# Kernel optimization log

Measured on AMD Instinct MI355X. Metric: run time of the kernel, lower is better.

The kernel has to match this reference:

```python
import jax, jax.numpy as jnp
import numpy as np

B, T, N_EMBD, H = 8, 2048, 1024, 128

def setup_inputs() -> dict:
    key = jax.random.key(0)
    k1, k2, k3, k4 = jax.random.split(key, 4)
    x = jax.random.normal(k1, (B, T, N_EMBD), dtype=jnp.float32)
    s = 1.0 / np.sqrt(N_EMBD).astype(np.float32)
    Wq = jax.random.normal(k2, (N_EMBD, H), dtype=jnp.float32) * s
    Wk = jax.random.normal(k3, (N_EMBD, H), dtype=jnp.float32) * s
    Wv = jax.random.normal(k4, (N_EMBD, H), dtype=jnp.float32) * s
    return {"x": x, "Wq": Wq, "Wk": Wk, "Wv": Wv}

def reference(x, Wq, Wk, Wv):
    # x: [B,T,C]; projections (no bias per init_kwargs)
    q = x @ Wq  # [B,T,H]
    k = x @ Wk  # [B,T,H]
    v = x @ Wv  # [B,T,H]
    scale = jnp.asarray(k.shape[-1], x.dtype) ** -0.5
    att = jnp.einsum('bth,bsh->bts', q, k) * scale  # [B,T,T]
    Tlen = x.shape[1]
    causal = jnp.tril(jnp.ones((Tlen, Tlen), dtype=bool))  # bias buffer tril mask
    att = jnp.where(causal, att, jnp.asarray(-jnp.inf, att.dtype))
    att = jax.nn.softmax(att, axis=-1)
    # dropout omitted (eval mode / deterministic reference)
    y = jnp.einsum('bts,bsh->bth', att, v)  # [B,T,H]
    return y
```

## Files before the change

kernel.cpp:

```cpp
#include <hip/hip_runtime.h>
#include <hip/hip_bf16.h>
#include <stdint.h>

#define BB 8
#define TT 2048
#define CC 1024
#define HH 128
#define VTP 2112

typedef __attribute__((ext_vector_type(8))) short bf16x8;
typedef __attribute__((ext_vector_type(8))) unsigned short u16x8;
typedef __attribute__((ext_vector_type(4))) float f32x4;
typedef __attribute__((ext_vector_type(8))) _Float16 h16x8;

static __device__ __forceinline__ unsigned short f2bf(float f) {
    union { float f; uint32_t u; } v; v.f = f;
    return (unsigned short)((v.u + 0x7fffu + ((v.u >> 16) & 1u)) >> 16);
}

#define GLOBAL_AS __attribute__((address_space(1)))
#define LDS_AS    __attribute__((address_space(3)))
static __device__ __forceinline__ void async16(const void* g, void* l) {
    __builtin_amdgcn_global_load_lds((const GLOBAL_AS void*)g, (LDS_AS void*)l, 16, 0, 0);
}

__global__ __launch_bounds__(256) void wconv(
    const float* __restrict__ Wq, const float* __restrict__ Wk,
    const float* __restrict__ Wv, unsigned short* __restrict__ Wb)
{
    int u = blockIdx.x * 256 + threadIdx.x;
    if (u >= 3 * 128 * 128) return;
    int kc = u & 127, n = (u >> 7) & 127, mat = u >> 14;
    const float* W = (mat == 0) ? Wq : (mat == 1) ? Wk : Wv;
    const float* s = W + (size_t)(kc * 8) * HH + n;
    u16x8 v;
    #pragma unroll
    for (int j = 0; j < 8; j++) v[j] = f2bf(s[(size_t)j * HH]);
    *(u16x8*)(Wb + ((size_t)mat * HH + n) * CC + kc * 8) = v;
}

#define BS_U16 2304
#define EQ_OFF 0
#define EK_OFF 4352
#define EV_OFF 8704
__global__ __launch_bounds__(256) void qkv_proj(
    const float* __restrict__ x, const unsigned short* __restrict__ Wb,
    unsigned short* __restrict__ Q, unsigned short* __restrict__ K,
    unsigned short* __restrict__ Vt)
{
    __shared__ __align__(16) unsigned short lds[26880];

    const int m0  = blockIdx.x * 32;
    const int tid = threadIdx.x;
    const int lane = tid & 63;
    const int w    = tid >> 6;
    const int qd   = lane >> 4;
    const int ln   = lane & 15;

    f32x4 acc[2][6];
    #pragma unroll
    for (int i = 0; i < 2; i++)
        #pragma unroll
        for (int j = 0; j < 6; j++) acc[i][j] = (f32x4){0.f,0.f,0.f,0.f};

    const int xr = tid >> 3;
    const int xg = (tid & 7) * 8;

    float4 xf[2];
    {
        const float* s = x + (size_t)(m0 + xr) * CC + xg;
        xf[0] = ((const float4*)s)[0];
        xf[1] = ((const float4*)s)[1];
    }

    for (int k0 = 0; k0 < CC; k0 += 64) {
        {
            u16x8 v0;
            v0[0]=f2bf(xf[0].x); v0[1]=f2bf(xf[0].y); v0[2]=f2bf(xf[0].z); v0[3]=f2bf(xf[0].w);
            v0[4]=f2bf(xf[1].x); v0[5]=f2bf(xf[1].y); v0[6]=f2bf(xf[1].z); v0[7]=f2bf(xf[1].w);
            *(u16x8*)&lds[xr * 72 + xg] = v0;
        }
        #pragma unroll
        for (int i = 0; i < 12; i++) {
            int sb = i * 256 + w * 64;
            int slot = sb + lane;
            int row = slot >> 3, j = (slot & 7) ^ (row & 7);
            async16(Wb + (size_t)row * CC + k0 + j * 8, &lds[BS_U16 + sb * 8]);
        }
        __syncthreads();
        if (k0 + 64 < CC) {
            const float* s = x + (size_t)(m0 + xr) * CC + k0 + 64 + xg;
            xf[0] = ((const float4*)s)[0];
            xf[1] = ((const float4*)s)[1];
        }
        #pragma unroll
        for (int ks = 0; ks < 2; ks++) {
            bf16x8 a0 = *(const bf16x8*)&lds[ln * 72 + ks*32 + qd*8];
            bf16x8 a1 = *(const bf16x8*)&lds[(16 + ln) * 72 + ks*32 + qd*8];
            #pragma unroll
            for (int nf = 0; nf < 6; nf++) {
                int row = w * 96 + nf * 16 + ln;
                int ch  = (ks * 4 + qd) ^ (row & 7);
                bf16x8 b = *(const bf16x8*)&lds[BS_U16 + (row * 8 + ch) * 8];
                acc[0][nf] = __builtin_amdgcn_mfma_f32_16x16x32_bf16(a0, b, acc[0][nf], 0, 0, 0);
                acc[1][nf] = __builtin_amdgcn_mfma_f32_16x16x32_bf16(a1, b, acc[1][nf], 0, 0, 0);
            }
        }
        __syncthreads();
    }

    #pragma unroll
    for (int mf = 0; mf < 2; mf++)
        #pragma unroll
        for (int nf = 0; nf < 6; nf++) {
            int n = w * 96 + nf * 16;
            int mat = n >> 7, hb = n & 127;
            #pragma unroll
            for (int r = 0; r < 4; r++) {
                unsigned short v = f2bf(acc[mf][nf][r]);
                int mrow = mf*16 + qd*4 + r;
                if (mat < 2) lds[(mat ? EK_OFF : EQ_OFF) + mrow * 136 + hb + ln] = v;
                else         lds[EV_OFF + (hb + ln) * 40 + mrow] = v;
            }
        }
    __syncthreads();
    {
        int rr = tid >> 3, c0 = (tid & 7) * 16;
        #pragma unroll
        for (int i = 0; i < 2; i++) {
            u16x8 vq = *(const u16x8*)&lds[EQ_OFF + rr * 136 + c0 + i * 8];
            *(u16x8*)(Q + (size_t)(m0 + rr) * HH + c0 + i * 8) = vq;
            u16x8 vk = *(const u16x8*)&lds[EK_OFF + rr * 136 + c0 + i * 8];
            *(u16x8*)(K + (size_t)(m0 + rr) * HH + c0 + i * 8) = vk;
        }
    }
    {
        int bb = m0 >> 11, t0 = m0 & (TT - 1);
        int hh = tid >> 1, tf = (tid & 1) * 16;
        #pragma unroll
        for (int i = 0; i < 2; i++) {
            u16x8 vv = *(const u16x8*)&lds[EV_OFF + hh * 40 + tf + i * 8];
            *(u16x8*)(Vt + ((size_t)bb * HH + hh) * VTP + t0 + tf + i * 8) = vv;
        }
    }
}

__global__ __launch_bounds__(256) void attn(
    const unsigned short* __restrict__ Q, const unsigned short* __restrict__ K,
    const unsigned short* __restrict__ Vt, float* __restrict__ out)
{
    __shared__ __align__(16) unsigned short Ks[2][64 * 128];
    __shared__ __align__(16) unsigned short Vs[2][128 * 64];
    __shared__ __align__(16) unsigned short Ps[4][16 * 40];
    __shared__ float Lp[4][16];

    const int tid  = threadIdx.x;
    const int lane = tid & 63;
    const int wave = tid >> 6;
    const int qd = lane >> 4;
    const int ln = lane & 15;
    const int qgrp  = wave >> 1;
    const int khalf = wave & 1;

    const int bx = blockIdx.x;
    int b, qt;
    if (bx < 256) { b = bx & 7;               qt = 63 - (bx >> 3); }
    else          { int u = bx - 256; b = u & 7; qt = u >> 3; }
    const int qbase = qt * 32 + qgrp * 16;
    const int nst = (qt + 2) >> 1;

    const unsigned short* Qb = Q  + (size_t)b * TT * HH;
    const unsigned short* Kb = K  + (size_t)b * TT * HH;
    const unsigned short* Vb = Vt + (size_t)b * HH * VTP;

    bf16x8 aq[4];
    #pragma unroll
    for (int c = 0; c < 4; c++)
        aq[c] = *(const bf16x8*)(Qb + (size_t)(qbase + ln) * HH + c * 32 + qd * 8);

    f32x4 O[8];
    float lsum[4];
    #pragma unroll
    for (int h = 0; h < 8; h++) O[h] = (f32x4){0.f,0.f,0.f,0.f};
    #pragma unroll
    for (int r = 0; r < 4; r++) lsum[r] = 0.f;

    const float sl   = 0.08838834764831843f * 1.4426950408889634f;
    const float M0L2 = 7.2134752044448f;
    unsigned short* ps = Ps[wave];

    #define STAGE(S0, BUF)                                                          \
        do {                                                                        \
            _Pragma("unroll")                                                       \
            for (int i = 0; i < 4; i++) {                                           \
                int sb = i * 256 + wave * 64;                                       \
                int slot = sb + lane;                                               \
                int row = slot >> 4, jj = (slot & 15) ^ (row & 15);                 \
                async16(Kb + (size_t)((S0) + row) * HH + jj * 8, &Ks[BUF][sb * 8]); \
            }                                                                       \
            _Pragma("unroll")                                                       \
            for (int i = 0; i < 4; i++) {                                           \
                int sb = i * 256 + wave * 64;                                       \
                int slot = sb + lane;                                               \
                int row = slot >> 3, jj = (slot & 7) ^ (row & 7);                   \
                async16(Vb + (size_t)row * VTP + (S0) + jj * 8, &Vs[BUF][sb * 8]);  \
            }                                                                       \
        } while (0)

    STAGE(0, 0);
    for (int st = 0; st < nst; st++) {
        __syncthreads();
        const int buf = st & 1;
        if (st + 1 < nst) STAGE((st + 1) * 64, buf ^ 1);
        const int s0 = st * 64;

        f32x4 s[2] = {(f32x4){0.f,0.f,0.f,0.f}, (f32x4){0.f,0.f,0.f,0.f}};
        #pragma unroll
        for (int nt = 0; nt < 2; nt++) {
            int krow = khalf * 32 + nt * 16;
            #pragma unroll
            for (int c = 0; c < 4; c++) {
                bf16x8 bk = *(const bf16x8*)&Ks[buf][(krow + ln) * 128 + ((c*4 + qd) ^ ln) * 8];
                s[nt] = __builtin_amdgcn_mfma_f32_16x16x32_bf16(aq[c], bk, s[nt], 0, 0, 0);
            }
        }
        #pragma unroll
        for (int nt = 0; nt < 2; nt++) {
            int col = s0 + khalf * 32 + nt * 16 + ln;
            #pragma unroll
            for (int r = 0; r < 4; r++) {
                int row = qbase + qd * 4 + r;
                float e = __builtin_amdgcn_exp2f(s[nt][r] * sl - M0L2);
                e = (col <= row) ? e : 0.f;
                lsum[r] += e;
                ps[(qd*4 + r) * 40 + nt*16 + ln] = f2bf(e);
            }
        }
        bf16x8 ap = *(const bf16x8*)&ps[ln * 40 + qd * 8];
        #pragma unroll
        for (int ht = 0; ht < 8; ht++) {
            int vrow = ht * 16 + ln;
            bf16x8 bv = *(const bf16x8*)&Vs[buf][vrow * 64 + ((khalf*4 + qd) ^ (vrow & 7)) * 8];
            O[ht] = __builtin_amdgcn_mfma_f32_16x16x32_bf16(ap, bv, O[ht], 0, 0, 0);
        }
    }

    __syncthreads();
    #pragma unroll
    for (int r = 0; r < 4; r++) {
        float sum = lsum[r];
        #pragma unroll
        for (int off = 1; off < 16; off <<= 1)
            sum += __shfl_xor(sum, off, 64);
        if (ln == 0) Lp[wave][qd*4 + r] = sum;
    }
    _Float16* om = (_Float16*)&Ks[0][0] + (size_t)wave * 16 * 128;
    #pragma unroll
    for (int ht = 0; ht < 8; ht++)
        #pragma unroll
        for (int r = 0; r < 4; r++)
            om[(qd*4 + r) * 128 + ht*16 + ln] = (_Float16)O[ht][r];
    __syncthreads();

    {
        int row = tid >> 3, h0 = (tid & 7) * 16;
        int g = row >> 4, q = row & 15;
        float L = Lp[2*g][q] + Lp[2*g + 1][q];
        float inv = 1.0f / L;
        const _Float16* p0 = (const _Float16*)&Ks[0][0] + (size_t)(2*g) * 2048 + q * 128 + h0;
        const _Float16* p1 = p0 + 2048;
        float* op = out + ((size_t)b * TT + qt * 32 + row) * HH + h0;
        #pragma unroll
        for (int i = 0; i < 4; i++) {
            float4 v;
            v.x = ((float)p0[i*4+0] + (float)p1[i*4+0]) * inv;
            v.y = ((float)p0[i*4+1] + (float)p1[i*4+1]) * inv;
            v.z = ((float)p0[i*4+2] + (float)p1[i*4+2]) * inv;
            v.w = ((float)p0[i*4+3] + (float)p1[i*4+3]) * inv;
            ((float4*)op)[i] = v;
        }
    }
    #undef STAGE
}

extern "C" void kernel_launch(void* const* d_in, const int* in_sizes, int n_in,
                              void* d_out, int out_size, void* d_ws, size_t ws_size,
                              hipStream_t stream) {
    const float* x  = (const float*)d_in[0];
    const float* Wq = (const float*)d_in[1];
    const float* Wk = (const float*)d_in[2];
    const float* Wv = (const float*)d_in[3];

    unsigned short* Wb = (unsigned short*)d_ws;
    unsigned short* Qw = Wb + (size_t)3 * HH * CC;
    unsigned short* Kw = Qw + (size_t)BB * TT * HH;
    unsigned short* Vw = Kw + (size_t)BB * TT * HH;

    wconv<<<dim3(192), 256, 0, stream>>>(Wq, Wk, Wv, Wb);
    qkv_proj<<<dim3(512), 256, 0, stream>>>(x, Wb, Qw, Kw, Vw);
    attn<<<dim3(512), 256, 0, stream>>>(Qw, Kw, Vw, (float*)d_out);
}
```

Baseline: 160.5 us.

## Split attention key range across four waves per query group, drop double buffering

The attention block grows from 256 to 512 threads, so each 16-row query group is processed by four waves instead of two, each covering a 32-key slice of a 128-key stage. K/V tiles are loaded once per 128-key stage into a single LDS buffer with a barrier before compute, replacing the previous double-buffered prefetch of 64-key stages. The epilogue sums four partial outputs and row sums. This halves the number of stages and raises the wave count per block, but gives up overlap of loads with compute and adds an extra barrier per stage. It also computes more fully masked work on the diagonal stage.

Measured after the change: 153.6 us. -4.3%, faster.

```diff
diff --git a/kernel.cpp b/kernel.cpp
--- a/kernel.cpp
+++ b/kernel.cpp
@@ -145,29 +145,30 @@
     }
 }
 
-__global__ __launch_bounds__(256) void attn(
+__global__ __launch_bounds__(512) void attn(
     const unsigned short* __restrict__ Q, const unsigned short* __restrict__ K,
     const unsigned short* __restrict__ Vt, float* __restrict__ out)
 {
-    __shared__ __align__(16) unsigned short Ks[2][64 * 128];
-    __shared__ __align__(16) unsigned short Vs[2][128 * 64];
-    __shared__ __align__(16) unsigned short Ps[4][16 * 40];
-    __shared__ float Lp[4][16];
+    __shared__ __align__(16) unsigned short Ks[128 * 128];
+    __shared__ __align__(16) unsigned short Vs[128 * 128];
+    __shared__ __align__(16) unsigned short Ps[8][16 * 40];
+    __shared__ float Lp[8][16];
 
     const int tid  = threadIdx.x;
     const int lane = tid & 63;
     const int wave = tid >> 6;
     const int qd = lane >> 4;
     const int ln = lane & 15;
-    const int qgrp  = wave >> 1;
-    const int khalf = wave & 1;
+    const int qgrp = wave >> 2;
+    const int kq   = wave & 2 ? (wave & 3) : (wave & 3);
+    const int kq4  = wave & 3;
 
     const int bx = blockIdx.x;
     int b, qt;
     if (bx < 256) { b = bx & 7;               qt = 63 - (bx >> 3); }
     else          { int u = bx - 256; b = u & 7; qt = u >> 3; }
     const int qbase = qt * 32 + qgrp * 16;
-    const int nst = (qt + 2) >> 1;
+    const int nst = (qt + 4) >> 2;
 
     const unsigned short* Qb = Q  + (size_t)b * TT * HH;
     const unsigned short* Kb = K  + (size_t)b * TT * HH;
@@ -189,44 +190,37 @@
     const float M0L2 = 7.2134752044448f;
     unsigned short* ps = Ps[wave];
 
-    #define STAGE(S0, BUF)                                                          \
-        do {                                                                        \
-            _Pragma("unroll")                                                       \
-            for (int i = 0; i < 4; i++) {                                           \
-                int sb = i * 256 + wave * 64;                                       \
-                int slot = sb + lane;                                               \
-                int row = slot >> 4, jj = (slot & 15) ^ (row & 15);                 \
-                async16(Kb + (size_t)((S0) + row) * HH + jj * 8, &Ks[BUF][sb * 8]); \
-            }                                                                       \
-            _Pragma("unroll")                                                       \
-            for (int i = 0; i < 4; i++) {                                           \
-                int sb = i * 256 + wave * 64;                                       \
-                int slot = sb + lane;                                               \
-                int row = slot >> 3, jj = (slot & 7) ^ (row & 7);                   \
-                async16(Vb + (size_t)row * VTP + (S0) + jj * 8, &Vs[BUF][sb * 8]);  \
-            }                                                                       \
-        } while (0)
-
-    STAGE(0, 0);
     for (int st = 0; st < nst; st++) {
+        const int s0 = st * 128;
+        #pragma unroll
+        for (int i = 0; i < 4; i++) {
+            int sb = i * 512 + wave * 64;
+            int slot = sb + lane;
+            int row = slot >> 4, jj = (slot & 15) ^ (row & 15);
+            async16(Kb + (size_t)(s0 + row) * HH + jj * 8, &Ks[sb * 8]);
+        }
+        #pragma unroll
+        for (int i = 0; i < 4; i++) {
+            int sb = i * 512 + wave * 64;
+            int slot = sb + lane;
+            int row = slot >> 4, jj = (slot & 15) ^ (row & 15);
+            async16(Vb + (size_t)row * VTP + s0 + jj * 8, &Vs[sb * 8]);
+        }
         __syncthreads();
-        const int buf = st & 1;
-        if (st + 1 < nst) STAGE((st + 1) * 64, buf ^ 1);
-        const int s0 = st * 64;
 
         f32x4 s[2] = {(f32x4){0.f,0.f,0.f,0.f}, (f32x4){0.f,0.f,0.f,0.f}};
         #pragma unroll
         for (int nt = 0; nt < 2; nt++) {
-            int krow = khalf * 32 + nt * 16;
+            int krow = kq4 * 32 + nt * 16;
             #pragma unroll
             for (int c = 0; c < 4; c++) {
-                bf16x8 bk = *(const bf16x8*)&Ks[buf][(krow + ln) * 128 + ((c*4 + qd) ^ ln) * 8];
+                bf16x8 bk = *(const bf16x8*)&Ks[(krow + ln) * 128 + (((c*4 + qd) ^ ln)) * 8];
                 s[nt] = __builtin_amdgcn_mfma_f32_16x16x32_bf16(aq[c], bk, s[nt], 0, 0, 0);
             }
         }
         #pragma unroll
         for (int nt = 0; nt < 2; nt++) {
-            int col = s0 + khalf * 32 + nt * 16 + ln;
+            int col = s0 + kq4 * 32 + nt * 16 + ln;
             #pragma unroll
             for (int r = 0; r < 4; r++) {
                 int row = qbase + qd * 4 + r;
@@ -240,9 +234,10 @@
         #pragma unroll
         for (int ht = 0; ht < 8; ht++) {
             int vrow = ht * 16 + ln;
-            bf16x8 bv = *(const bf16x8*)&Vs[buf][vrow * 64 + ((khalf*4 + qd) ^ (vrow & 7)) * 8];
+            bf16x8 bv = *(const bf16x8*)&Vs[vrow * 128 + (((kq4*4 + qd) ^ ln)) * 8];
             O[ht] = __builtin_amdgcn_mfma_f32_16x16x32_bf16(ap, bv, O[ht], 0, 0, 0);
         }
+        if (st + 1 < nst) __syncthreads();
     }
 
     __syncthreads();
@@ -254,7 +249,7 @@
             sum += __shfl_xor(sum, off, 64);
         if (ln == 0) Lp[wave][qd*4 + r] = sum;
     }
-    _Float16* om = (_Float16*)&Ks[0][0] + (size_t)wave * 16 * 128;
+    _Float16* om = (_Float16*)&Ks[0] + (size_t)wave * 16 * 128;
     #pragma unroll
     for (int ht = 0; ht < 8; ht++)
         #pragma unroll
@@ -263,24 +258,25 @@
     __syncthreads();
 
     {
-        int row = tid >> 3, h0 = (tid & 7) * 16;
+        int row = tid >> 4, h0 = (tid & 15) * 8;
         int g = row >> 4, q = row & 15;
-        float L = Lp[2*g][q] + Lp[2*g + 1][q];
+        float L = Lp[g*4 + 0][q] + Lp[g*4 + 1][q] + Lp[g*4 + 2][q] + Lp[g*4 + 3][q];
         float inv = 1.0f / L;
-        const _Float16* p0 = (const _Float16*)&Ks[0][0] + (size_t)(2*g) * 2048 + q * 128 + h0;
+        const _Float16* p0 = (const _Float16*)&Ks[0] + (size_t)(g*4 + 0) * 2048 + q * 128 + h0;
         const _Float16* p1 = p0 + 2048;
+        const _Float16* p2 = p1 + 2048;
+        const _Float16* p3 = p2 + 2048;
         float* op = out + ((size_t)b * TT + qt * 32 + row) * HH + h0;
         #pragma unroll
-        for (int i = 0; i < 4; i++) {
+        for (int i = 0; i < 2; i++) {
             float4 v;
-            v.x = ((float)p0[i*4+0] + (float)p1[i*4+0]) * inv;
-            v.y = ((float)p0[i*4+1] + (float)p1[i*4+1]) * inv;
-            v.z = ((float)p0[i*4+2] + (float)p1[i*4+2]) * inv;
-            v.w = ((float)p0[i*4+3] + (float)p1[i*4+3]) * inv;
+            v.x = (((float)p0[i*4+0] + (float)p1[i*4+0]) + ((float)p2[i*4+0] + (float)p3[i*4+0])) * inv;
+            v.y = (((float)p0[i*4+1] + (float)p1[i*4+1]) + ((float)p2[i*4+1] + (float)p3[i*4+1])) * inv;
+            v.z = (((float)p0[i*4+2] + (float)p1[i*4+2]) + ((float)p2[i*4+2] + (float)p3[i*4+2])) * inv;
+            v.w = (((float)p0[i*4+3] + (float)p1[i*4+3]) + ((float)p2[i*4+3] + (float)p3[i*4+3])) * inv;
             ((float4*)op)[i] = v;
         }
     }
-    #undef STAGE
 }
 
 extern "C" void kernel_launch(void* const* d_in, const int* in_sizes, int n_in,
@@ -298,5 +294,5 @@
 
     wconv<<<dim3(192), 256, 0, stream>>>(Wq, Wk, Wv, Wb);
     qkv_proj<<<dim3(512), 256, 0, stream>>>(x, Wb, Qw, Kw, Vw);
-    attn<<<dim3(512), 256, 0, stream>>>(Qw, Kw, Vw, (float*)d_out);
-}
+    attn<<<dim3(512), 512, 0, stream>>>(Qw, Kw, Vw, (float*)d_out);
+}
```
